# Optimization experiments

Hardware: AMD Instinct MI355X
Metric: run time of the kernel (lower is better)

## Reference

```python
import jax, jax.numpy as jnp
import numpy as np

LATENT = 768
HEADS = 12
HEAD_DIM = LATENT // HEADS
FFN = 4 * LATENT


def setup_inputs() -> dict:
    key = jax.random.key(0)
    ks = jax.random.split(key, 16)
    s = 1.0 / np.sqrt(LATENT)
    inp = {
        "x": jax.random.normal(ks[0], (2, 2048, LATENT), dtype=jnp.float32),
        "Wq": jax.random.normal(ks[1], (LATENT, LATENT), dtype=jnp.float32) * s,
        "bq": jnp.zeros((LATENT,), jnp.float32),
        "Wk": jax.random.normal(ks[2], (LATENT, LATENT), dtype=jnp.float32) * s,
        "bk": jnp.zeros((LATENT,), jnp.float32),
        "Wv": jax.random.normal(ks[3], (LATENT, LATENT), dtype=jnp.float32) * s,
        "bv": jnp.zeros((LATENT,), jnp.float32),
        "Wo": jax.random.normal(ks[4], (LATENT, LATENT), dtype=jnp.float32) * s,
        "bo": jnp.zeros((LATENT,), jnp.float32),
        "ln1_g": jnp.ones((LATENT,), jnp.float32),
        "ln1_b": jnp.zeros((LATENT,), jnp.float32),
        "ln2_g": jnp.ones((LATENT,), jnp.float32),
        "ln2_b": jnp.zeros((LATENT,), jnp.float32),
        "W1": jax.random.normal(ks[5], (FFN, LATENT), dtype=jnp.float32) * s,
        "b1": jnp.zeros((FFN,), jnp.float32),
        "W2": jax.random.normal(ks[6], (LATENT, FFN), dtype=jnp.float32) * (1.0 / np.sqrt(FFN)),
        "b2": jnp.zeros((LATENT,), jnp.float32),
    }
    return inp


def _layernorm(x, g, b, eps=1e-5):
    mu = jnp.mean(x, axis=-1, keepdims=True)
    var = jnp.var(x, axis=-1, keepdims=True)
    return (x - mu) * jax.lax.rsqrt(var + eps) * g + b


def reference(x, Wq, bq, Wk, bk, Wv, bv, Wo, bo, ln1_g, ln1_b, ln2_g, ln2_b, W1, b1, W2, b2):
    b, n, d = x.shape
    # torch Linear: y = x @ W.T + bias
    Q = (x @ Wq.T + bq).reshape(b, n, HEADS, HEAD_DIM).transpose(0, 2, 1, 3)
    K = (x @ Wk.T + bk).reshape(b, n, HEADS, HEAD_DIM).transpose(0, 2, 1, 3)
    V = (x @ Wv.T + bv).reshape(b, n, HEADS, HEAD_DIM).transpose(0, 2, 1, 3)
    scores = jnp.einsum("bhqd,bhkd->bhqk", Q, K) / np.sqrt(HEAD_DIM)  # [b,h,n,n]
    weights = jax.nn.softmax(scores, axis=-1)
    attn = jnp.einsum("bhqk,bhkd->bhqd", weights, V)
    attn = attn.transpose(0, 2, 1, 3).reshape(b, n, d)
    attn = attn @ Wo.T + bo
    x = _layernorm(x + attn, ln1_g, ln1_b)
    h = jax.nn.gelu(x @ W1.T + b1, approximate=False)
    ffn = h @ W2.T + b2
    x = _layernorm(x + ffn, ln2_g, ln2_b)
    return x
```

## Files before the change

### kernel.cpp

```cpp
#include <hip/hip_runtime.h>
#include <hip/hip_bf16.h>
#include <cstddef>
#include <cstdint>

typedef __bf16 bf16_t;
typedef bf16_t bf16x8 __attribute__((ext_vector_type(8)));
typedef bf16_t bf16x4 __attribute__((ext_vector_type(4)));
typedef float f32x4 __attribute__((ext_vector_type(4)));

#define LATENT 768
#define FFN_DIM 3072
#define NTOK 4096
#define SEQ 2048
#define HEADS 12
#define HD 64

#define C2F 0.18033688011112042f

__device__ __forceinline__ void gload_lds16(const bf16_t* g, bf16_t* l) {
    __builtin_amdgcn_global_load_lds((const __attribute__((address_space(1))) void*)g,
                                     (__attribute__((address_space(3))) void*)l, 16, 0, 0);
}

struct CvtDesc {
    const float* src[7];
    bf16_t* dst[7];
    int n4[7];
    const float* bsrc[3];
    float* bdst;
};

__global__ __launch_bounds__(256) void cvt_f32_bf16(CvtDesc d) {
    int seg = blockIdx.y;
    if (seg == 7) {
        int which = blockIdx.x;
        if (which >= 3) return;
        int t = threadIdx.x;
#pragma unroll
        for (int i = 0; i < 3; ++i)
            d.bdst[which * LATENT + t + i * 256] = d.bsrc[which][t + i * 256];
        return;
    }
    int i = blockIdx.x * 256 + threadIdx.x;
    if (i >= d.n4[seg]) return;
    float4 v = ((const float4*)d.src[seg])[i];
    bf16x4 o;
    o[0] = (bf16_t)v.x; o[1] = (bf16_t)v.y; o[2] = (bf16_t)v.z; o[3] = (bf16_t)v.w;
    *(bf16x4*)&d.dst[seg][(size_t)i * 4] = o;
}

template<int EPI>
__global__ __launch_bounds__(512) void gemm128(const bf16_t* __restrict__ A,
                                               const bf16_t* __restrict__ B,
                                               const float* __restrict__ bias,
                                               void* __restrict__ Cv,
                                               int M, int N, int K) {
    __shared__ __align__(16) bf16_t As[2][128 * 32];
    __shared__ __align__(16) bf16_t Bs[2][128 * 32];
    int t = threadIdx.x;
    int w = t >> 6;
    int lane = t & 63, l16 = lane & 15, quad = lane >> 4;
    int xt = blockIdx.x + blockIdx.y;
    if (xt >= (int)gridDim.x) xt -= gridDim.x;
    int m0 = xt * 128, n0 = blockIdx.y * 128;
    int wm = w & 1, wn = w >> 1;
    int mrow0 = wm * 64, ncol0 = wn * 32;

    f32x4 acc[4][2] = {};

    int srow = lane >> 2;
    int sseg = (lane & 3) * 8;

    auto stage = [&](int k0, int buf) {
        const bf16_t* Ag = A + (size_t)(m0 + w * 16 + srow) * K + k0 + sseg;
        gload_lds16(Ag, &As[buf][(w * 16) * 32]);
        const bf16_t* Bg = B + (size_t)(n0 + w * 16 + srow) * K + k0 + sseg;
        gload_lds16(Bg, &Bs[buf][(w * 16) * 32]);
    };

    int niter = K / 32;
    stage(0, 0);
    for (int kt = 0; kt < niter; ++kt) {
        __syncthreads();
        int cur = kt & 1;
        if (kt + 1 < niter) stage((kt + 1) * 32, cur ^ 1);

        bf16x8 a[4], b[2];
#pragma unroll
        for (int i = 0; i < 4; ++i)
            a[i] = *(const bf16x8*)&As[cur][(mrow0 + i * 16 + l16) * 32 + quad * 8];
#pragma unroll
        for (int j = 0; j < 2; ++j)
            b[j] = *(const bf16x8*)&Bs[cur][(ncol0 + j * 16 + l16) * 32 + quad * 8];
#pragma unroll
        for (int i = 0; i < 4; ++i)
#pragma unroll
            for (int j = 0; j < 2; ++j)
                acc[i][j] = __builtin_amdgcn_mfma_f32_16x16x32_bf16(a[i], b[j], acc[i][j], 0, 0, 0);
    }

    float* Cf = (float*)Cv;
    bf16_t* Cb = (bf16_t*)Cv;
#pragma unroll
    for (int j = 0; j < 2; ++j) {
        int col = n0 + ncol0 + j * 16 + l16;
        float bvv = bias[col];
#pragma unroll
        for (int i = 0; i < 4; ++i) {
            int row0 = m0 + mrow0 + i * 16 + quad * 4;
#pragma unroll
            for (int r = 0; r < 4; ++r) {
                float v = acc[i][j][r] + bvv;
                if (EPI == 2) v = 0.5f * v * (1.0f + erff(v * 0.70710678118654752f));
                if (EPI == 3) { if (col < LATENT) v *= C2F; }
                if (EPI == 0) Cf[(size_t)(row0 + r) * N + col] = v;
                else          Cb[(size_t)(row0 + r) * N + col] = (bf16_t)v;
            }
        }
    }
}

template<int EPI>
__global__ __launch_bounds__(256) void gemm64(const bf16_t* __restrict__ A,
                                              const bf16_t* __restrict__ B,
                                              const float* __restrict__ bias,
                                              void* __restrict__ Cv,
                                              int M, int N, int K) {
    __shared__ __align__(16) bf16_t As[2][64 * 32];
    __shared__ __align__(16) bf16_t Bs[2][64 * 32];
    int t = threadIdx.x;
    int w = t >> 6;
    int lane = t & 63, l16 = lane & 15, quad = lane >> 4;
    int m0 = blockIdx.x * 64, n0 = blockIdx.y * 64;
    int wm = w & 1, wn = w >> 1;

    f32x4 acc[2][2] = {};

    int srow = lane >> 2;
    int sseg = (lane & 3) * 8;

    auto stage = [&](int k0, int buf) {
        const bf16_t* Ag = A + (size_t)(m0 + w * 16 + srow) * K + k0 + sseg;
        gload_lds16(Ag, &As[buf][(w * 16) * 32]);
        const bf16_t* Bg = B + (size_t)(n0 + w * 16 + srow) * K + k0 + sseg;
        gload_lds16(Bg, &Bs[buf][(w * 16) * 32]);
    };

    int niter = K / 32;
    stage(0, 0);
    for (int kt = 0; kt < niter; ++kt) {
        __syncthreads();
        int cur = kt & 1;
        if (kt + 1 < niter) stage((kt + 1) * 32, cur ^ 1);

        bf16x8 a[2], b[2];
#pragma unroll
        for (int i = 0; i < 2; ++i)
            a[i] = *(const bf16x8*)&As[cur][(wm * 32 + i * 16 + l16) * 32 + quad * 8];
#pragma unroll
        for (int j = 0; j < 2; ++j)
            b[j] = *(const bf16x8*)&Bs[cur][(wn * 32 + j * 16 + l16) * 32 + quad * 8];
#pragma unroll
        for (int i = 0; i < 2; ++i)
#pragma unroll
            for (int j = 0; j < 2; ++j)
                acc[i][j] = __builtin_amdgcn_mfma_f32_16x16x32_bf16(a[i], b[j], acc[i][j], 0, 0, 0);
    }

    float* Cf = (float*)Cv;
    bf16_t* Cb = (bf16_t*)Cv;
#pragma unroll
    for (int j = 0; j < 2; ++j) {
        int col = n0 + wn * 32 + j * 16 + l16;
        float bvv = bias[col];
#pragma unroll
        for (int i = 0; i < 2; ++i) {
            int row0 = m0 + wm * 32 + i * 16 + quad * 4;
#pragma unroll
            for (int r = 0; r < 4; ++r) {
                float v = acc[i][j][r] + bvv;
                if (EPI == 2) v = 0.5f * v * (1.0f + erff(v * 0.70710678118654752f));
                if (EPI == 0) Cf[(size_t)(row0 + r) * N + col] = v;
                else          Cb[(size_t)(row0 + r) * N + col] = (bf16_t)v;
            }
        }
    }
}

__global__ __launch_bounds__(256) void v_transpose(const bf16_t* __restrict__ QKV,
                                                   bf16_t* __restrict__ Vt) {
    __shared__ bf16_t Ts[64][68];
    int t = threadIdx.x;
    int bh = blockIdx.y;
    int b = bh / HEADS, h = bh % HEADS;
    int n0 = blockIdx.x * 64;
    size_t rowbase = (size_t)b * SEQ;
    int r = t >> 3, seg = (t & 7) * 8;
#pragma unroll
    for (int i = 0; i < 2; ++i) {
        int rr = r + i * 32;
        *(bf16x8*)&Ts[rr][seg] =
            *(const bf16x8*)&QKV[(rowbase + n0 + rr) * (3 * LATENT) + 2 * LATENT + h * HD + seg];
    }
    __syncthreads();
#pragma unroll
    for (int i = 0; i < 2; ++i) {
        int d = r + i * 32;
        bf16x8 o;
#pragma unroll
        for (int jj = 0; jj < 8; ++jj) o[jj] = Ts[seg + jj][d];
        *(bf16x8*)&Vt[((size_t)bh * HD + d) * SEQ + n0 + seg] = o;
    }
}

__global__ __launch_bounds__(256) void attn_flash(const bf16_t* __restrict__ QKV,
                                                  const bf16_t* __restrict__ Vt,
                                                  float* __restrict__ Op0,
                                                  float* __restrict__ Op1,
                                                  float* __restrict__ vs0,
                                                  float* __restrict__ vs1) {
    __shared__ __align__(16) bf16_t Ks[2][2][64][32];
    __shared__ __align__(16) bf16_t Vts[2][2][64][32];
    __shared__ __align__(16) bf16_t Ps[4][32][72];

    int t = threadIdx.x;
    int w = t >> 6;
    int lane = t & 63, l16 = lane & 15, quad = lane >> 4;
    int bh = blockIdx.x;
    int b = bh / HEADS, h = bh % HEADS;
    int qblk = blockIdx.y * 128;
    int z = blockIdx.z;
    float* Op = z ? Op1 : Op0;
    float* vs = z ? vs1 : vs0;
    size_t rowbase = (size_t)b * SEQ;
    int kbase = z * (SEQ / 2);
    const int LD = 3 * LATENT;
    int qw = qblk + w * 32;

    bf16x8 bq[2][2];
#pragma unroll
    for (int qt = 0; qt < 2; ++qt) {
        const bf16_t* qrow = QKV + (rowbase + qw + qt * 16 + l16) * LD + h * HD;
        bq[qt][0] = *(const bf16x8*)&qrow[quad * 8];
        bq[qt][1] = *(const bf16x8*)&qrow[32 + quad * 8];
    }

    f32x4 acc[2][4] = {};
    float vsum[2] = {};

    int srow = lane >> 2;
    int sseg = (lane & 3) * 8;

    {
        const bf16_t* kg = QKV + (rowbase + kbase + w * 16 + srow) * LD + LATENT + h * HD + sseg;
        gload_lds16(kg,      &Ks[0][0][w * 16][0]);
        gload_lds16(kg + 32, &Ks[0][1][w * 16][0]);
        const bf16_t* vg = Vt + ((size_t)bh * HD + w * 16 + srow) * SEQ + kbase + sseg;
        gload_lds16(vg,      &Vts[0][0][w * 16][0]);
        gload_lds16(vg + 32, &Vts[0][1][w * 16][0]);
    }

    for (int kt = 0; kt < SEQ / 128; ++kt) {
        __syncthreads();
        int cur = kt & 1;
        if (kt + 1 < SEQ / 128) {
            int nxt = cur ^ 1;
            int koff = kbase + (kt + 1) * 64;
            const bf16_t* kg = QKV + (rowbase + koff + w * 16 + srow) * LD + LATENT + h * HD + sseg;
            gload_lds16(kg,      &Ks[nxt][0][w * 16][0]);
            gload_lds16(kg + 32, &Ks[nxt][1][w * 16][0]);
            const bf16_t* vg = Vt + ((size_t)bh * HD + w * 16 + srow) * SEQ + koff + sseg;
            gload_lds16(vg,      &Vts[nxt][0][w * 16][0]);
            gload_lds16(vg + 32, &Vts[nxt][1][w * 16][0]);
        }

#pragma unroll
        for (int skt = 0; skt < 4; ++skt) {
            bf16x8 ak0 = *(const bf16x8*)&Ks[cur][0][skt * 16 + l16][quad * 8];
            bf16x8 ak1 = *(const bf16x8*)&Ks[cur][1][skt * 16 + l16][quad * 8];
#pragma unroll
            for (int qt = 0; qt < 2; ++qt) {
                f32x4 s = {};
                s = __builtin_amdgcn_mfma_f32_16x16x32_bf16(ak0, bq[qt][0], s, 0, 0, 0);
                s = __builtin_amdgcn_mfma_f32_16x16x32_bf16(ak1, bq[qt][1], s, 0, 0, 0);
                bf16x4 pk;
#pragma unroll
                for (int r = 0; r < 4; ++r) {
                    float p = __builtin_amdgcn_exp2f(s[r]);
                    vsum[qt] += p;
                    pk[r] = (bf16_t)p;
                }
                *(bf16x4*)&Ps[w][qt * 16 + l16][skt * 16 + quad * 4] = pk;
            }
        }
        __threadfence_block();

        bf16x8 bv[4][2];
#pragma unroll
        for (int dt = 0; dt < 4; ++dt) {
            bv[dt][0] = *(const bf16x8*)&Vts[cur][0][dt * 16 + l16][quad * 8];
            bv[dt][1] = *(const bf16x8*)&Vts[cur][1][dt * 16 + l16][quad * 8];
        }
#pragma unroll
        for (int qt = 0; qt < 2; ++qt) {
#pragma unroll
            for (int kc = 0; kc < 2; ++kc) {
                bf16x8 ap = *(const bf16x8*)&Ps[w][qt * 16 + l16][kc * 32 + quad * 8];
#pragma unroll
                for (int dt = 0; dt < 4; ++dt)
                    acc[qt][dt] = __builtin_amdgcn_mfma_f32_16x16x32_bf16(ap, bv[dt][kc], acc[qt][dt], 0, 0, 0);
            }
        }
    }

#pragma unroll
    for (int qt = 0; qt < 2; ++qt) {
        vsum[qt] += __shfl_xor(vsum[qt], 16, 64);
        vsum[qt] += __shfl_xor(vsum[qt], 32, 64);
        if (quad == 0)
            vs[(rowbase + qw + qt * 16 + l16) * HEADS + h] = vsum[qt];
    }

#pragma unroll
    for (int qt = 0; qt < 2; ++qt)
#pragma unroll
        for (int dt = 0; dt < 4; ++dt)
#pragma unroll
            for (int r = 0; r < 4; ++r) {
                size_t row = rowbase + qw + qt * 16 + quad * 4 + r;
                Op[row * LATENT + h * HD + dt * 16 + l16] = acc[qt][dt][r];
            }
}

__global__ __launch_bounds__(256) void attn_combine(const float* __restrict__ Op0,
                                                    const float* __restrict__ Op1,
                                                    const float* __restrict__ vs0,
                                                    const float* __restrict__ vs1,
                                                    bf16_t* __restrict__ O) {
    int row = blockIdx.x;
    int t = threadIdx.x;
    const float* a = Op0 + (size_t)row * LATENT;
    const float* bb = Op1 + (size_t)row * LATENT;
#pragma unroll
    for (int i = 0; i < 3; ++i) {
        int c = t + i * 256;
        int h = c >> 6;
        float denom = vs0[(size_t)row * HEADS + h] + vs1[(size_t)row * HEADS + h];
        O[(size_t)row * LATENT + c] = (bf16_t)((a[c] + bb[c]) / denom);
    }
}

__global__ __launch_bounds__(256) void ln_residual(const float* __restrict__ base,
                                                   const float* __restrict__ add,
                                                   const float* __restrict__ g,
                                                   const float* __restrict__ bta,
                                                   float* __restrict__ outf,
                                                   bf16_t* __restrict__ outb) {
    int row = blockIdx.x;
    const float* xr = base + (size_t)row * LATENT;
    const float* ar = add + (size_t)row * LATENT;
    int t = threadIdx.x;
    float v[3];
    float s = 0.f;
#pragma unroll
    for (int i = 0; i < 3; ++i) {
        v[i] = xr[t + i * 256] + ar[t + i * 256];
        s += v[i];
    }
    __shared__ float red[4];
#pragma unroll
    for (int off = 1; off < 64; off <<= 1) s += __shfl_xor(s, off, 64);
    if ((t & 63) == 0) red[t >> 6] = s;
    __syncthreads();
    float mu = (red[0] + red[1] + red[2] + red[3]) * (1.f / LATENT);
    float q = 0.f;
#pragma unroll
    for (int i = 0; i < 3; ++i) {
        float d = v[i] - mu;
        q += d * d;
    }
#pragma unroll
    for (int off = 1; off < 64; off <<= 1) q += __shfl_xor(q, off, 64);
    __syncthreads();
    if ((t & 63) == 0) red[t >> 6] = q;
    __syncthreads();
    float var = (red[0] + red[1] + red[2] + red[3]) * (1.f / LATENT);
    float rs = rsqrtf(var + 1e-5f);
#pragma unroll
    for (int i = 0; i < 3; ++i) {
        int cix = t + i * 256;
        float o = (v[i] - mu) * rs * g[cix] + bta[cix];
        outf[(size_t)row * LATENT + cix] = o;
        if (outb) outb[(size_t)row * LATENT + cix] = (bf16_t)o;
    }
}

extern "C" void kernel_launch(void* const* d_in, const int* in_sizes, int n_in,
                              void* d_out, int out_size, void* d_ws, size_t ws_size,
                              hipStream_t stream) {
    const float* x   = (const float*)d_in[0];
    const float* Wq  = (const float*)d_in[1];
    const float* bq  = (const float*)d_in[2];
    const float* Wk  = (const float*)d_in[3];
    const float* bk  = (const float*)d_in[4];
    const float* Wv  = (const float*)d_in[5];
    const float* bv  = (const float*)d_in[6];
    const float* Wo  = (const float*)d_in[7];
    const float* bo  = (const float*)d_in[8];
    const float* g1  = (const float*)d_in[9];
    const float* be1 = (const float*)d_in[10];
    const float* g2  = (const float*)d_in[11];
    const float* be2 = (const float*)d_in[12];
    const float* W1  = (const float*)d_in[13];
    const float* b1  = (const float*)d_in[14];
    const float* W2  = (const float*)d_in[15];
    const float* b2  = (const float*)d_in[16];
    float* out = (float*)d_out;

    char* ws = (char*)d_ws;
    size_t off = 0;
    auto alloc = [&](size_t bytes) {
        char* p = ws + off;
        off = (off + bytes + 255) & ~(size_t)255;
        return p;
    };
    bf16_t* xbf   = (bf16_t*)alloc((size_t)NTOK * LATENT * 2);
    bf16_t* Wcat  = (bf16_t*)alloc((size_t)3 * LATENT * LATENT * 2);
    bf16_t* Wobf  = (bf16_t*)alloc((size_t)LATENT * LATENT * 2);
    bf16_t* W1bf  = (bf16_t*)alloc((size_t)FFN_DIM * LATENT * 2);
    bf16_t* W2bf  = (bf16_t*)alloc((size_t)LATENT * FFN_DIM * 2);
    float*  bcat  = (float*)alloc((size_t)3 * LATENT * 4);
    bf16_t* QKV   = (bf16_t*)alloc((size_t)NTOK * 3 * LATENT * 2);
    bf16_t* attnO = (bf16_t*)alloc((size_t)NTOK * LATENT * 2);
    float*  tmpf  = (float*)alloc((size_t)NTOK * LATENT * 4);
    float*  y1f   = (float*)alloc((size_t)NTOK * LATENT * 4);
    bf16_t* y1bf  = (bf16_t*)alloc((size_t)NTOK * LATENT * 2);
    bf16_t* hbf   = (bf16_t*)alloc((size_t)NTOK * FFN_DIM * 2);
    float*  vsa   = (float*)alloc((size_t)NTOK * HEADS * 4);
    float*  vsb   = (float*)alloc((size_t)NTOK * HEADS * 4);
    bf16_t* Vtg   = (bf16_t*)hbf;
    float*  Oa    = tmpf;
    float*  Ob    = y1f;

    CvtDesc cd;
    cd.src[0] = x;   cd.dst[0] = xbf;                        cd.n4[0] = NTOK * LATENT / 4;
    cd.src[1] = Wq;  cd.dst[1] = Wcat;                       cd.n4[1] = LATENT * LATENT / 4;
    cd.src[2] = Wk;  cd.dst[2] = Wcat + LATENT * LATENT;     cd.n4[2] = LATENT * LATENT / 4;
    cd.src[3] = Wv;  cd.dst[3] = Wcat + 2 * LATENT * LATENT; cd.n4[3] = LATENT * LATENT / 4;
    cd.src[4] = Wo;  cd.dst[4] = Wobf;                       cd.n4[4] = LATENT * LATENT / 4;
    cd.src[5] = W1;  cd.dst[5] = W1bf;                       cd.n4[5] = FFN_DIM * LATENT / 4;
    cd.src[6] = W2;  cd.dst[6] = W2bf;                       cd.n4[6] = FFN_DIM * LATENT / 4;
    cd.bsrc[0] = bq; cd.bsrc[1] = bk; cd.bsrc[2] = bv;
    cd.bdst = bcat;
    {
        int maxn4 = NTOK * LATENT / 4;
        dim3 grid((maxn4 + 255) / 256, 8);
        cvt_f32_bf16<<<grid, 256, 0, stream>>>(cd);
    }

    gemm128<3><<<dim3(NTOK / 128, 3 * LATENT / 128), 512, 0, stream>>>(
        xbf, Wcat, bcat, QKV, NTOK, 3 * LATENT, LATENT);

    v_transpose<<<dim3(SEQ / 64, 2 * HEADS), 256, 0, stream>>>(QKV, Vtg);

    attn_flash<<<dim3(2 * HEADS, SEQ / 128, 2), 256, 0, stream>>>(QKV, Vtg, Oa, Ob, vsa, vsb);

    attn_combine<<<NTOK, 256, 0, stream>>>(Oa, Ob, vsa, vsb, attnO);

    gemm64<0><<<dim3(NTOK / 64, LATENT / 64), 256, 0, stream>>>(
        attnO, Wobf, bo, tmpf, NTOK, LATENT, LATENT);

    ln_residual<<<NTOK, 256, 0, stream>>>(x, tmpf, g1, be1, y1f, y1bf);

    gemm128<2><<<dim3(NTOK / 128, FFN_DIM / 128), 512, 0, stream>>>(
        y1bf, W1bf, b1, hbf, NTOK, FFN_DIM, LATENT);

    gemm64<0><<<dim3(NTOK / 64, LATENT / 64), 256, 0, stream>>>(
        hbf, W2bf, b2, tmpf, NTOK, LATENT, FFN_DIM);

    ln_residual<<<NTOK, 256, 0, stream>>>(y1f, tmpf, g2, be2, out, nullptr);
}
```

Measured before the change: 302.1 us.

## Split-K the FFN down-projection GEMM and reduce partials in LayerNorm

Replaces the 64x64-tile W2 GEMM (K=3072, only 384 blocks) with a 128x128-tile split-K kernel that divides K into four slices, writing four fp32 partial outputs into reused workspace buffers. The final residual LayerNorm is templated to sum those partials before normalizing. The goal is more parallelism and larger tiles for the long-K GEMM. The cost is extra fp32 partial-sum traffic (four NTOK x LATENT buffers written and read) and one extra workspace buffer.

```diff
diff --git a/kernel.cpp b/kernel.cpp
--- a/kernel.cpp
+++ b/kernel.cpp
@@ -116,6 +116,73 @@
                 if (EPI == 0) Cf[(size_t)(row0 + r) * N + col] = v;
                 else          Cb[(size_t)(row0 + r) * N + col] = (bf16_t)v;
             }
+        }
+    }
+}
+
+struct SKDst { float* p[4]; };
+
+__global__ __launch_bounds__(512) void gemm128sk(const bf16_t* __restrict__ A,
+                                                 const bf16_t* __restrict__ B,
+                                                 const float* __restrict__ bias,
+                                                 SKDst dst,
+                                                 int M, int N, int Ktot) {
+    __shared__ __align__(16) bf16_t As[2][128 * 32];
+    __shared__ __align__(16) bf16_t Bs[2][128 * 32];
+    int t = threadIdx.x;
+    int w = t >> 6;
+    int lane = t & 63, l16 = lane & 15, quad = lane >> 4;
+    int z = blockIdx.z;
+    int KS = Ktot >> 2;
+    int kbase = z * KS;
+    int m0 = blockIdx.x * 128, n0 = blockIdx.y * 128;
+    int wm = w & 1, wn = w >> 1;
+    int mrow0 = wm * 64, ncol0 = wn * 32;
+
+    f32x4 acc[4][2] = {};
+
+    int srow = lane >> 2;
+    int sseg = (lane & 3) * 8;
+
+    auto stage = [&](int k0, int buf) {
+        const bf16_t* Ag = A + (size_t)(m0 + w * 16 + srow) * Ktot + kbase + k0 + sseg;
+        gload_lds16(Ag, &As[buf][(w * 16) * 32]);
+        const bf16_t* Bg = B + (size_t)(n0 + w * 16 + srow) * Ktot + kbase + k0 + sseg;
+        gload_lds16(Bg, &Bs[buf][(w * 16) * 32]);
+    };
+
+    int niter = KS / 32;
+    stage(0, 0);
+    for (int kt = 0; kt < niter; ++kt) {
+        __syncthreads();
+        int cur = kt & 1;
+        if (kt + 1 < niter) stage((kt + 1) * 32, cur ^ 1);
+
+        bf16x8 a[4], b[2];
+#pragma unroll
+        for (int i = 0; i < 4; ++i)
+            a[i] = *(const bf16x8*)&As[cur][(mrow0 + i * 16 + l16) * 32 + quad * 8];
+#pragma unroll
+        for (int j = 0; j < 2; ++j)
+            b[j] = *(const bf16x8*)&Bs[cur][(ncol0 + j * 16 + l16) * 32 + quad * 8];
+#pragma unroll
+        for (int i = 0; i < 4; ++i)
+#pragma unroll
+            for (int j = 0; j < 2; ++j)
+                acc[i][j] = __builtin_amdgcn_mfma_f32_16x16x32_bf16(a[i], b[j], acc[i][j], 0, 0, 0);
+    }
+
+    float* Cf = dst.p[z];
+#pragma unroll
+    for (int j = 0; j < 2; ++j) {
+        int col = n0 + ncol0 + j * 16 + l16;
+        float bvv = (z == 0) ? bias[col] : 0.f;
+#pragma unroll
+        for (int i = 0; i < 4; ++i) {
+            int row0 = m0 + mrow0 + i * 16 + quad * 4;
+#pragma unroll
+            for (int r = 0; r < 4; ++r)
+                Cf[(size_t)(row0 + r) * N + col] = acc[i][j][r] + bvv;
         }
     }
 }
@@ -350,22 +417,30 @@
     }
 }
 
+template<int NADD>
 __global__ __launch_bounds__(256) void ln_residual(const float* __restrict__ base,
-                                                   const float* __restrict__ add,
+                                                   const float* __restrict__ a1,
+                                                   const float* __restrict__ a2,
+                                                   const float* __restrict__ a3,
+                                                   const float* __restrict__ a4,
                                                    const float* __restrict__ g,
                                                    const float* __restrict__ bta,
                                                    float* __restrict__ outf,
                                                    bf16_t* __restrict__ outb) {
     int row = blockIdx.x;
-    const float* xr = base + (size_t)row * LATENT;
-    const float* ar = add + (size_t)row * LATENT;
+    size_t ro = (size_t)row * LATENT;
     int t = threadIdx.x;
     float v[3];
     float s = 0.f;
 #pragma unroll
     for (int i = 0; i < 3; ++i) {
-        v[i] = xr[t + i * 256] + ar[t + i * 256];
-        s += v[i];
+        int cix = t + i * 256;
+        float x = base[ro + cix] + a1[ro + cix];
+        if (NADD >= 2) x += a2[ro + cix];
+        if (NADD >= 3) x += a3[ro + cix];
+        if (NADD >= 4) x += a4[ro + cix];
+        v[i] = x;
+        s += x;
     }
     __shared__ float red[4];
 #pragma unroll
@@ -390,8 +465,8 @@
     for (int i = 0; i < 3; ++i) {
         int cix = t + i * 256;
         float o = (v[i] - mu) * rs * g[cix] + bta[cix];
-        outf[(size_t)row * LATENT + cix] = o;
-        if (outb) outb[(size_t)row * LATENT + cix] = (bf16_t)o;
+        outf[ro + cix] = o;
+        if (outb) outb[ro + cix] = (bf16_t)o;
     }
 }
 
@@ -438,9 +513,13 @@
     bf16_t* hbf   = (bf16_t*)alloc((size_t)NTOK * FFN_DIM * 2);
     float*  vsa   = (float*)alloc((size_t)NTOK * HEADS * 4);
     float*  vsb   = (float*)alloc((size_t)NTOK * HEADS * 4);
+    float*  P3    = (float*)alloc((size_t)NTOK * LATENT * 4);
     bf16_t* Vtg   = (bf16_t*)hbf;
     float*  Oa    = tmpf;
     float*  Ob    = y1f;
+    float* P0 = tmpf;
+    float* P1 = (float*)QKV;
+    float* P2 = (float*)xbf;
 
     CvtDesc cd;
     cd.src[0] = x;   cd.dst[0] = xbf;                        cd.n4[0] = NTOK * LATENT / 4;
@@ -470,13 +549,17 @@
     gemm64<0><<<dim3(NTOK / 64, LATENT / 64), 256, 0, stream>>>(
         attnO, Wobf, bo, tmpf, NTOK, LATENT, LATENT);
 
-    ln_residual<<<NTOK, 256, 0, stream>>>(x, tmpf, g1, be1, y1f, y1bf);
+    ln_residual<1><<<NTOK, 256, 0, stream>>>(x, tmpf, nullptr, nullptr, nullptr,
+                                             g1, be1, y1f, y1bf);
 
     gemm128<2><<<dim3(NTOK / 128, FFN_DIM / 128), 512, 0, stream>>>(
         y1bf, W1bf, b1, hbf, NTOK, FFN_DIM, LATENT);
 
-    gemm64<0><<<dim3(NTOK / 64, LATENT / 64), 256, 0, stream>>>(
-        hbf, W2bf, b2, tmpf, NTOK, LATENT, FFN_DIM);
-
-    ln_residual<<<NTOK, 256, 0, stream>>>(y1f, tmpf, g2, be2, out, nullptr);
-}
+    SKDst skd;
+    skd.p[0] = P0; skd.p[1] = P1; skd.p[2] = P2; skd.p[3] = P3;
+    gemm128sk<<<dim3(NTOK / 128, LATENT / 128, 4), 512, 0, stream>>>(
+        hbf, W2bf, b2, skd, NTOK, LATENT, FFN_DIM);
+
+    ln_residual<4><<<NTOK, 256, 0, stream>>>(y1f, P0, P1, P2, P3,
+                                             g2, be2, out, nullptr);
+}
```

Result: faster. 294.8 us (-2.4%).
